# Performance work log

Measured on AMD Instinct MI355X. Metric: run time of the kernel, lower is better.

Reference implementation:

```python
import jax, jax.numpy as jnp
import numpy as np

B, T, D, R = 4, 2048, 1024, 32


def setup_inputs() -> dict:
    key = jax.random.key(0)
    kx, ku = jax.random.split(key)
    x = jax.random.normal(kx, (B, T, D), dtype=jnp.float32)
    # low-rank metric factor; small init so distances are moderate
    U = jax.random.normal(ku, (D, R), dtype=jnp.float32) * 0.05
    return {"x": x, "U": U}


def reference(x, U):
    # g = U @ U.T (PSD low-rank metric).
    # dist_sq[b,t,j] = (x_t - x_j)^T g (x_t - x_j)
    #               = ||U^T x_t||^2 + ||U^T x_j||^2 - 2 (U^T x_t).(U^T x_j)
    # Algebraic expansion of the original O(B*T*T*D) broadcasted diff tensor.
    y = jnp.einsum('btd,dr->btr', x, U)                # [B,T,R]
    n = jnp.sum(y * y, axis=-1)                         # [B,T]
    cross = jnp.einsum('btr,bjr->btj', y, y)            # [B,T,T]
    dist_sq = n[:, :, None] + n[:, None, :] - 2.0 * cross
    attn = jax.nn.softmax(-dist_sq, axis=-1)            # [B,T,T]
    return jnp.einsum('btj,bjd->btd', attn, x)          # [B,T,D]
```

## Files before the change

### kernel.cpp

```cpp
#include <hip/hip_runtime.h>

#define B_ 4
#define T_ 2048
#define D_ 1024
#define R_ 32
#define XSTR2 136

typedef __attribute__((ext_vector_type(8))) short short8;
typedef __attribute__((ext_vector_type(4))) float f32x4;
typedef __attribute__((ext_vector_type(4))) unsigned short us4;
typedef __attribute__((ext_vector_type(8))) unsigned short us8;

__device__ __forceinline__ unsigned short f2bf(float f) {
  union { float f; unsigned u; } v; v.f = f;
  unsigned r = (v.u + 0x7fffu + ((v.u >> 16) & 1u)) >> 16;
  return (unsigned short)r;
}
__device__ __forceinline__ float bf2f(unsigned short h) {
  union { unsigned u; float f; } v; v.u = (unsigned)h << 16;
  return v.f;
}

__global__ __launch_bounds__(256)
void geo_ut(const float* __restrict__ U, unsigned short* __restrict__ Ut) {
  __shared__ float tile[128][33];
  const int tid = threadIdx.x;
  const int d0 = blockIdx.x * 128;
  #pragma unroll
  for (int i = 0; i < 16; i++) {
    int e = i * 256 + tid;
    int d = e >> 5, r = e & 31;
    tile[d][r] = U[(size_t)(d0 + d) * R_ + r];
  }
  __syncthreads();
  const int r = tid >> 3, seg = tid & 7;
  us8 o0, o1;
  #pragma unroll
  for (int k = 0; k < 8; k++) o0[k] = f2bf(tile[seg * 16 + k][r]);
  #pragma unroll
  for (int k = 0; k < 8; k++) o1[k] = f2bf(tile[seg * 16 + 8 + k][r]);
  *(us8*)(Ut + (size_t)r * D_ + d0 + seg * 16) = o0;
  *(us8*)(Ut + (size_t)r * D_ + d0 + seg * 16 + 8) = o1;
}

__global__ __launch_bounds__(256)
void geo_prep(const float* __restrict__ x, const unsigned short* __restrict__ Ut,
              unsigned short* __restrict__ xt, float* __restrict__ y_part) {
  __shared__ unsigned short xs[2][32 * XSTR2];
  const int b = blockIdx.y, slab = blockIdx.z;
  const int t0 = blockIdx.x * 32;
  const int d0 = slab * 256;
  const int tid = threadIdx.x, w = tid >> 6, lane = tid & 63;
  const int m = lane & 15, quad = lane >> 4;
  const int Mt = w & 1, Nt = w >> 1;
  const int lr = tid >> 3;
  const int lc = (tid & 7) * 16;

  const float* xb = x + ((size_t)b * T_ + t0 + lr) * D_ + d0 + lc;
  float4 v[2][4];
  #pragma unroll
  for (int ch = 0; ch < 2; ch++)
    #pragma unroll
    for (int i = 0; i < 4; i++)
      v[ch][i] = *(const float4*)(xb + ch * 128 + i * 4);
  #pragma unroll
  for (int ch = 0; ch < 2; ch++)
    #pragma unroll
    for (int i = 0; i < 4; i++) {
      us4 c;
      c[0] = f2bf(v[ch][i].x); c[1] = f2bf(v[ch][i].y);
      c[2] = f2bf(v[ch][i].z); c[3] = f2bf(v[ch][i].w);
      *(us4*)&xs[ch][lr * XSTR2 + lc + i * 4] = c;
    }
  __syncthreads();
  {
    const int wd = tid >> 1, wt = (tid & 1) * 16;
    #pragma unroll
    for (int ch = 0; ch < 2; ch++) {
      us8 o0, o1;
      #pragma unroll
      for (int k = 0; k < 8; k++) {
        o0[k] = xs[ch][(wt + k) * XSTR2 + wd];
        o1[k] = xs[ch][(wt + 8 + k) * XSTR2 + wd];
      }
      unsigned short* xo = xt + ((size_t)b * D_ + d0 + ch * 128 + wd) * T_ + t0;
      *(us8*)(xo + wt) = o0;
      *(us8*)(xo + wt + 8) = o1;
    }
  }
  f32x4 acc = {0.f, 0.f, 0.f, 0.f};
  #pragma unroll
  for (int ch = 0; ch < 2; ch++)
    #pragma unroll
    for (int ks = 0; ks < 4; ks++) {
      short8 af = *(const short8*)&xs[ch][(Mt * 16 + m) * XSTR2 + ks * 32 + quad * 8];
      short8 bf = *(const short8*)(Ut + (size_t)(Nt * 16 + m) * D_ + d0 + ch * 128 + ks * 32 + quad * 8);
      acc = __builtin_amdgcn_mfma_f32_16x16x32_bf16(af, bf, acc, 0, 0, 0);
    }
  float* yp = y_part + ((size_t)(slab * B_ + b) * T_ + t0 + Mt * 16 + quad * 4) * R_ + Nt * 16 + m;
  #pragma unroll
  for (int k = 0; k < 4; k++) yp[(size_t)k * R_] = acc[k];
}

__global__ __launch_bounds__(256)
void geo_reduce(const float* __restrict__ y_part, unsigned short* __restrict__ ybf,
                float* __restrict__ nsq, float* __restrict__ l) {
  const int tid = threadIdx.x;
  const size_t row = (size_t)blockIdx.x * 32 + (tid >> 3);
  const int r0 = (tid & 7) * 4;
  f32x4 v = {0.f, 0.f, 0.f, 0.f};
  #pragma unroll
  for (int s = 0; s < 4; s++) {
    f32x4 p = *(const f32x4*)(y_part + ((size_t)s * B_ * T_ + row) * R_ + r0);
    #pragma unroll
    for (int k = 0; k < 4; k++) v[k] += p[k];
  }
  us4 pk;
  float part = 0.f;
  #pragma unroll
  for (int k = 0; k < 4; k++) {
    pk[k] = f2bf(1.41421356237f * v[k]);
    float b = bf2f(pk[k]);
    part += b * b;
  }
  *(us4*)(ybf + row * R_ + r0) = pk;
  part += __shfl_xor(part, 1, 64);
  part += __shfl_xor(part, 2, 64);
  part += __shfl_xor(part, 4, 64);
  if ((tid & 7) == 0) { nsq[row] = 0.5f * part; l[row] = 0.f; }
}

__global__ __launch_bounds__(256)
void geo_scores(const unsigned short* __restrict__ ybf,
                const float* __restrict__ nsq,
                unsigned short* __restrict__ P, float* __restrict__ l,
                int jg0, int Kslab) {
  const int b = blockIdx.z;
  const int t0 = blockIdx.x * 128;
  const int jl0 = blockIdx.y * 128;
  const int tid = threadIdx.x, w = tid >> 6, lane = tid & 63;
  const int m = lane & 15, quad = lane >> 4;
  const unsigned short* yb = ybf + (size_t)b * T_ * R_;
  const float* nb = nsq + b * T_;
  const int jw = jl0 + w * 32;
  short8 aj[2]; f32x4 njv[2];
  #pragma unroll
  for (int rb = 0; rb < 2; rb++) {
    aj[rb] = *(const short8*)(yb + (size_t)(jg0 + jw + rb * 16 + m) * R_ + quad * 8);
    njv[rb] = *(const f32x4*)(nb + jg0 + jw + rb * 16 + quad * 4);
  }
  unsigned short* Pb = P + (size_t)b * T_ * Kslab;
  short8 btn = *(const short8*)(yb + (size_t)(t0 + m) * R_ + quad * 8);
  float ntn = nb[t0 + m];
  #pragma unroll 2
  for (int cb = 0; cb < 8; cb++) {
    const int t = t0 + cb * 16 + m;
    short8 bt = btn;
    float nt = ntn;
    if (cb < 7) {
      btn = *(const short8*)(yb + (size_t)(t + 16) * R_ + quad * 8);
      ntn = nb[t + 16];
    }
    float ls = 0.f;
    #pragma unroll
    for (int rb = 0; rb < 2; rb++) {
      f32x4 z = {0.f, 0.f, 0.f, 0.f};
      f32x4 c = __builtin_amdgcn_mfma_f32_16x16x32_bf16(aj[rb], bt, z, 0, 0, 0);
      us4 pk;
      #pragma unroll
      for (int r = 0; r < 4; r++) {
        float p = __expf(c[r] - njv[rb][r] - nt);
        ls += p;
        pk[r] = f2bf(p);
      }
      *(us4*)(Pb + (size_t)t * Kslab + jw + rb * 16 + quad * 4) = pk;
    }
    ls += __shfl_xor(ls, 16, 64);
    ls += __shfl_xor(ls, 32, 64);
    if (quad == 0) atomicAdd(&l[b * T_ + t], ls);
  }
}

__global__ __launch_bounds__(256)
void geo_pv(const unsigned short* __restrict__ P,
            const unsigned short* __restrict__ xt,
            const float* __restrict__ l, float* __restrict__ out,
            int Kslab, int kxt0, int accumulate, int normalize) {
  __shared__ unsigned short As[128 * 64];
  __shared__ unsigned short Bs[128 * 64];
  const int b = blockIdx.z;
  const int id = blockIdx.x;
  const int cls = id & 7, kk = id >> 3;
  const int t0 = (2 * cls + (kk >> 3)) * 128;
  const int d0 = (kk & 7) * 128;
  const int tid = threadIdx.x, w = tid >> 6, lane = tid & 63;
  const int m = lane & 15, quad = lane >> 4;
  const int wr = (w & 1) * 64, wc = (w >> 1) * 64;
  const int srow = lane >> 3, sslot = lane & 7;
  const unsigned short* Pb = P + ((size_t)b * T_ + t0) * Kslab;
  const unsigned short* Xb = xt + ((size_t)b * D_ + d0) * T_ + kxt0;
  f32x4 acc[4][4];
  #pragma unroll
  for (int i = 0; i < 4; i++)
    #pragma unroll
    for (int j = 0; j < 4; j++) acc[i][j] = (f32x4){0.f, 0.f, 0.f, 0.f};

  for (int k0 = 0; k0 < Kslab; k0 += 64) {
    __syncthreads();
    #pragma unroll
    for (int cc = 0; cc < 4; cc++) {
      const int row = w * 32 + cc * 8 + srow;
      const int gs = sslot ^ (row & 7);
      __builtin_amdgcn_global_load_lds(
          (const __attribute__((address_space(1))) void*)(Pb + (size_t)row * Kslab + k0 + gs * 8),
          (__attribute__((address_space(3))) void*)(As + (w * 32 + cc * 8) * 64),
          16, 0, 0);
      __builtin_amdgcn_global_load_lds(
          (const __attribute__((address_space(1))) void*)(Xb + (size_t)row * T_ + k0 + gs * 8),
          (__attribute__((address_space(3))) void*)(Bs + (w * 32 + cc * 8) * 64),
          16, 0, 0);
    }
    __syncthreads();
    #pragma unroll
    for (int ks = 0; ks < 2; ks++) {
      short8 af[4], bf[4];
      #pragma unroll
      for (int i = 0; i < 4; i++) {
        const int ra = wr + i * 16 + m;
        af[i] = *(const short8*)(As + ra * 64 + (((ks * 4 + quad) ^ (m & 7)) * 8));
        const int cd = wc + i * 16 + m;
        bf[i] = *(const short8*)(Bs + cd * 64 + (((ks * 4 + quad) ^ (m & 7)) * 8));
      }
      #pragma unroll
      for (int rb = 0; rb < 4; rb++)
        #pragma unroll
        for (int cb = 0; cb < 4; cb++)
          acc[rb][cb] = __builtin_amdgcn_mfma_f32_16x16x32_bf16(af[rb], bf[cb], acc[rb][cb], 0, 0, 0);
    }
  }
  float* ob = out + ((size_t)b * T_ + t0 + wr) * D_ + d0 + wc;
  #pragma unroll
  for (int rb = 0; rb < 4; rb++) {
    f32x4 lv = *(const f32x4*)(l + b * T_ + t0 + wr + rb * 16 + quad * 4);
    f32x4 inv;
    #pragma unroll
    for (int r = 0; r < 4; r++) inv[r] = 1.f / lv[r];
    #pragma unroll
    for (int cb = 0; cb < 4; cb++) {
      #pragma unroll
      for (int r = 0; r < 4; r++) {
        float* p = ob + (size_t)(rb * 16 + quad * 4 + r) * D_ + cb * 16 + m;
        float v = acc[rb][cb][r];
        if (accumulate) v += *p;
        if (normalize) v *= inv[r];
        *p = v;
      }
    }
  }
}

extern "C" void kernel_launch(void* const* d_in, const int* in_sizes, int n_in,
                              void* d_out, int out_size, void* d_ws, size_t ws_size,
                              hipStream_t stream) {
  const float* x = (const float*)d_in[0];
  const float* U = (const float*)d_in[1];
  float* out = (float*)d_out;

  const size_t xt_b  = (size_t)B_ * D_ * T_ * 2;
  const size_t ybf_b = (size_t)B_ * T_ * R_ * 2;
  const size_t nsq_b = (size_t)B_ * T_ * 4;
  const size_t l_b   = nsq_b;
  const size_t ut_b  = (size_t)D_ * R_ * 2;
  const size_t yp_b  = (size_t)4 * B_ * T_ * R_ * 4;
  const size_t base  = xt_b + ybf_b + nsq_b + l_b + ut_b + yp_b;
  const size_t pfull = (size_t)B_ * T_ * T_ * 2;

  int nslab = 16;
  const int cand[5] = {1, 2, 4, 8, 16};
  for (int i = 0; i < 5; i++)
    if (base + pfull / (size_t)cand[i] <= ws_size) { nslab = cand[i]; break; }
  const int Kslab = T_ / nslab;

  char* wp = (char*)d_ws;
  unsigned short* xtp = (unsigned short*)wp;                 wp += xt_b;
  unsigned short* ybf = (unsigned short*)wp;                 wp += ybf_b;
  float* nsq = (float*)wp;                                   wp += nsq_b;
  float* lp  = (float*)wp;                                   wp += l_b;
  unsigned short* Utp = (unsigned short*)wp;                 wp += ut_b;
  float* ypart = (float*)wp;                                 wp += yp_b;
  unsigned short* P = (unsigned short*)wp;

  hipLaunchKernelGGL(geo_ut, dim3(D_ / 128), dim3(256), 0, stream, U, Utp);
  hipLaunchKernelGGL(geo_prep, dim3(T_ / 32, B_, 4), dim3(256), 0, stream,
                     x, Utp, xtp, ypart);
  hipLaunchKernelGGL(geo_reduce, dim3(B_ * T_ / 32), dim3(256), 0, stream,
                     ypart, ybf, nsq, lp);
  for (int s = 0; s < nslab; s++) {
    hipLaunchKernelGGL(geo_scores, dim3(T_ / 128, Kslab / 128, B_), dim3(256), 0, stream,
                       ybf, nsq, P, lp, s * Kslab, Kslab);
    hipLaunchKernelGGL(geo_pv, dim3(128, 1, B_), dim3(256), 0, stream,
                       P, xtp, lp, out, Kslab, s * Kslab,
                       (int)(s > 0), (int)(s == nslab - 1));
  }
}
```

Before: 156.5 us.

## Fuse score computation and softmax into PV GEMM, dropping materialized P matrix

Replaces the separate scores kernel, which wrote a bf16 probability matrix to global memory, with a single fused kernel. That kernel recomputes the exp scores per 64-column tile straight into shared memory and feeds them to the PV MFMA loop. Row sums are accumulated in registers and normalization happens in the epilogue, which removes the atomics, the P round trip and the multi-slab launches. The y vectors are prescaled by sqrt(2/ln2) so that exp2 can be used. The cost is that each of the eight d-tile blocks per t-tile recomputes the same scores, which adds redundant MFMA and exp work.

```diff
diff --git a/kernel.cpp b/kernel.cpp
--- a/kernel.cpp
+++ b/kernel.cpp
@@ -104,7 +104,7 @@
 
 __global__ __launch_bounds__(256)
 void geo_reduce(const float* __restrict__ y_part, unsigned short* __restrict__ ybf,
-                float* __restrict__ nsq, float* __restrict__ l) {
+                float* __restrict__ nsq) {
   const int tid = threadIdx.x;
   const size_t row = (size_t)blockIdx.x * 32 + (tid >> 3);
   const int r0 = (tid & 7) * 4;
@@ -119,7 +119,7 @@
   float part = 0.f;
   #pragma unroll
   for (int k = 0; k < 4; k++) {
-    pk[k] = f2bf(1.41421356237f * v[k]);
+    pk[k] = f2bf(1.69864446f * v[k]);
     float b = bf2f(pk[k]);
     part += b * b;
   }
@@ -127,98 +127,92 @@
   part += __shfl_xor(part, 1, 64);
   part += __shfl_xor(part, 2, 64);
   part += __shfl_xor(part, 4, 64);
-  if ((tid & 7) == 0) { nsq[row] = 0.5f * part; l[row] = 0.f; }
-}
-
-__global__ __launch_bounds__(256)
-void geo_scores(const unsigned short* __restrict__ ybf,
-                const float* __restrict__ nsq,
-                unsigned short* __restrict__ P, float* __restrict__ l,
-                int jg0, int Kslab) {
-  const int b = blockIdx.z;
-  const int t0 = blockIdx.x * 128;
-  const int jl0 = blockIdx.y * 128;
-  const int tid = threadIdx.x, w = tid >> 6, lane = tid & 63;
-  const int m = lane & 15, quad = lane >> 4;
-  const unsigned short* yb = ybf + (size_t)b * T_ * R_;
-  const float* nb = nsq + b * T_;
-  const int jw = jl0 + w * 32;
-  short8 aj[2]; f32x4 njv[2];
-  #pragma unroll
-  for (int rb = 0; rb < 2; rb++) {
-    aj[rb] = *(const short8*)(yb + (size_t)(jg0 + jw + rb * 16 + m) * R_ + quad * 8);
-    njv[rb] = *(const f32x4*)(nb + jg0 + jw + rb * 16 + quad * 4);
-  }
-  unsigned short* Pb = P + (size_t)b * T_ * Kslab;
-  short8 btn = *(const short8*)(yb + (size_t)(t0 + m) * R_ + quad * 8);
-  float ntn = nb[t0 + m];
-  #pragma unroll 2
-  for (int cb = 0; cb < 8; cb++) {
-    const int t = t0 + cb * 16 + m;
-    short8 bt = btn;
-    float nt = ntn;
-    if (cb < 7) {
-      btn = *(const short8*)(yb + (size_t)(t + 16) * R_ + quad * 8);
-      ntn = nb[t + 16];
-    }
-    float ls = 0.f;
-    #pragma unroll
-    for (int rb = 0; rb < 2; rb++) {
-      f32x4 z = {0.f, 0.f, 0.f, 0.f};
-      f32x4 c = __builtin_amdgcn_mfma_f32_16x16x32_bf16(aj[rb], bt, z, 0, 0, 0);
-      us4 pk;
-      #pragma unroll
-      for (int r = 0; r < 4; r++) {
-        float p = __expf(c[r] - njv[rb][r] - nt);
-        ls += p;
-        pk[r] = f2bf(p);
-      }
-      *(us4*)(Pb + (size_t)t * Kslab + jw + rb * 16 + quad * 4) = pk;
-    }
-    ls += __shfl_xor(ls, 16, 64);
-    ls += __shfl_xor(ls, 32, 64);
-    if (quad == 0) atomicAdd(&l[b * T_ + t], ls);
-  }
-}
-
-__global__ __launch_bounds__(256)
-void geo_pv(const unsigned short* __restrict__ P,
-            const unsigned short* __restrict__ xt,
-            const float* __restrict__ l, float* __restrict__ out,
-            int Kslab, int kxt0, int accumulate, int normalize) {
+  if ((tid & 7) == 0) nsq[row] = 0.5f * part;
+}
+
+__global__ __launch_bounds__(256, 2)
+void geo_fused(const unsigned short* __restrict__ ybf,
+               const float* __restrict__ nsq,
+               const unsigned short* __restrict__ xt,
+               float* __restrict__ out) {
   __shared__ unsigned short As[128 * 64];
   __shared__ unsigned short Bs[128 * 64];
+  __shared__ float l_s[128];
   const int b = blockIdx.z;
   const int id = blockIdx.x;
-  const int cls = id & 7, kk = id >> 3;
-  const int t0 = (2 * cls + (kk >> 3)) * 128;
-  const int d0 = (kk & 7) * 128;
+  const int d0 = (id & 7) * 128;
+  const int t0 = (id >> 3) * 128;
   const int tid = threadIdx.x, w = tid >> 6, lane = tid & 63;
   const int m = lane & 15, quad = lane >> 4;
   const int wr = (w & 1) * 64, wc = (w >> 1) * 64;
   const int srow = lane >> 3, sslot = lane & 7;
-  const unsigned short* Pb = P + ((size_t)b * T_ + t0) * Kslab;
-  const unsigned short* Xb = xt + ((size_t)b * D_ + d0) * T_ + kxt0;
+  const int tw = w * 32;
+
+  const unsigned short* yb = ybf + (size_t)b * T_ * R_;
+  const float* nb = nsq + b * T_;
+  const unsigned short* Xb = xt + ((size_t)b * D_ + d0) * T_;
+
+  short8 at[2]; float nnt[2]; float lsum[2] = {0.f, 0.f};
+  #pragma unroll
+  for (int tb = 0; tb < 2; tb++) {
+    at[tb] = *(const short8*)(yb + (size_t)(t0 + tw + tb * 16 + m) * R_ + quad * 8);
+    nnt[tb] = -nb[t0 + tw + tb * 16 + m];
+  }
+
   f32x4 acc[4][4];
   #pragma unroll
   for (int i = 0; i < 4; i++)
     #pragma unroll
     for (int j = 0; j < 4; j++) acc[i][j] = (f32x4){0.f, 0.f, 0.f, 0.f};
 
-  for (int k0 = 0; k0 < Kslab; k0 += 64) {
+  short8 aj[4]; f32x4 njv[4];
+  #pragma unroll
+  for (int ja = 0; ja < 4; ja++) {
+    aj[ja] = *(const short8*)(yb + (size_t)(ja * 16 + m) * R_ + quad * 8);
+    njv[ja] = *(const f32x4*)(nb + ja * 16 + quad * 4);
+  }
+
+  for (int j0 = 0; j0 < T_; j0 += 64) {
     __syncthreads();
     #pragma unroll
     for (int cc = 0; cc < 4; cc++) {
       const int row = w * 32 + cc * 8 + srow;
       const int gs = sslot ^ (row & 7);
       __builtin_amdgcn_global_load_lds(
-          (const __attribute__((address_space(1))) void*)(Pb + (size_t)row * Kslab + k0 + gs * 8),
-          (__attribute__((address_space(3))) void*)(As + (w * 32 + cc * 8) * 64),
-          16, 0, 0);
-      __builtin_amdgcn_global_load_lds(
-          (const __attribute__((address_space(1))) void*)(Xb + (size_t)row * T_ + k0 + gs * 8),
+          (const __attribute__((address_space(1))) void*)(Xb + (size_t)row * T_ + j0 + gs * 8),
           (__attribute__((address_space(3))) void*)(Bs + (w * 32 + cc * 8) * 64),
           16, 0, 0);
+    }
+    short8 caj[4]; f32x4 cnj[4];
+    #pragma unroll
+    for (int ja = 0; ja < 4; ja++) { caj[ja] = aj[ja]; cnj[ja] = njv[ja]; }
+    const int jn = (j0 + 64 < T_) ? j0 + 64 : 0;
+    #pragma unroll
+    for (int ja = 0; ja < 4; ja++) {
+      aj[ja] = *(const short8*)(yb + (size_t)(jn + ja * 16 + m) * R_ + quad * 8);
+      njv[ja] = *(const f32x4*)(nb + jn + ja * 16 + quad * 4);
+    }
+    #pragma unroll
+    for (int tb = 0; tb < 2; tb++) {
+      const int trow = tw + tb * 16 + m;
+      #pragma unroll
+      for (int ja = 0; ja < 4; ja++) {
+        f32x4 cin;
+        #pragma unroll
+        for (int r = 0; r < 4; r++) cin[r] = nnt[tb] - cnj[ja][r];
+        f32x4 c = __builtin_amdgcn_mfma_f32_16x16x32_bf16(caj[ja], at[tb], cin, 0, 0, 0);
+        us4 pk; float ls = 0.f;
+        #pragma unroll
+        for (int r = 0; r < 4; r++) {
+          float p = __builtin_amdgcn_exp2f(c[r]);
+          ls += p;
+          pk[r] = f2bf(p);
+        }
+        lsum[tb] += ls;
+        const int sb = ja * 2 + (quad >> 1);
+        char* dst = (char*)As + trow * 128 + ((sb ^ (trow & 7)) * 16) + (quad & 1) * 8;
+        *(us4*)dst = pk;
+      }
     }
     __syncthreads();
     #pragma unroll
@@ -238,24 +232,25 @@
           acc[rb][cb] = __builtin_amdgcn_mfma_f32_16x16x32_bf16(af[rb], bf[cb], acc[rb][cb], 0, 0, 0);
     }
   }
+  #pragma unroll
+  for (int tb = 0; tb < 2; tb++) {
+    lsum[tb] += __shfl_xor(lsum[tb], 16, 64);
+    lsum[tb] += __shfl_xor(lsum[tb], 32, 64);
+  }
+  if (quad == 0) { l_s[tw + m] = lsum[0]; l_s[tw + 16 + m] = lsum[1]; }
+  __syncthreads();
   float* ob = out + ((size_t)b * T_ + t0 + wr) * D_ + d0 + wc;
   #pragma unroll
   for (int rb = 0; rb < 4; rb++) {
-    f32x4 lv = *(const f32x4*)(l + b * T_ + t0 + wr + rb * 16 + quad * 4);
+    f32x4 lv = *(const f32x4*)&l_s[wr + rb * 16 + quad * 4];
     f32x4 inv;
     #pragma unroll
     for (int r = 0; r < 4; r++) inv[r] = 1.f / lv[r];
     #pragma unroll
-    for (int cb = 0; cb < 4; cb++) {
-      #pragma unroll
-      for (int r = 0; r < 4; r++) {
-        float* p = ob + (size_t)(rb * 16 + quad * 4 + r) * D_ + cb * 16 + m;
-        float v = acc[rb][cb][r];
-        if (accumulate) v += *p;
-        if (normalize) v *= inv[r];
-        *p = v;
-      }
-    }
+    for (int cb = 0; cb < 4; cb++)
+      #pragma unroll
+      for (int r = 0; r < 4; r++)
+        ob[(size_t)(rb * 16 + quad * 4 + r) * D_ + cb * 16 + m] = acc[rb][cb][r] * inv[r];
   }
 }
 
@@ -269,37 +264,22 @@
   const size_t xt_b  = (size_t)B_ * D_ * T_ * 2;
   const size_t ybf_b = (size_t)B_ * T_ * R_ * 2;
   const size_t nsq_b = (size_t)B_ * T_ * 4;
-  const size_t l_b   = nsq_b;
   const size_t ut_b  = (size_t)D_ * R_ * 2;
   const size_t yp_b  = (size_t)4 * B_ * T_ * R_ * 4;
-  const size_t base  = xt_b + ybf_b + nsq_b + l_b + ut_b + yp_b;
-  const size_t pfull = (size_t)B_ * T_ * T_ * 2;
-
-  int nslab = 16;
-  const int cand[5] = {1, 2, 4, 8, 16};
-  for (int i = 0; i < 5; i++)
-    if (base + pfull / (size_t)cand[i] <= ws_size) { nslab = cand[i]; break; }
-  const int Kslab = T_ / nslab;
 
   char* wp = (char*)d_ws;
   unsigned short* xtp = (unsigned short*)wp;                 wp += xt_b;
   unsigned short* ybf = (unsigned short*)wp;                 wp += ybf_b;
   float* nsq = (float*)wp;                                   wp += nsq_b;
-  float* lp  = (float*)wp;                                   wp += l_b;
   unsigned short* Utp = (unsigned short*)wp;                 wp += ut_b;
   float* ypart = (float*)wp;                                 wp += yp_b;
-  unsigned short* P = (unsigned short*)wp;
+  (void)ws_size; (void)in_sizes; (void)n_in; (void)out_size;
 
   hipLaunchKernelGGL(geo_ut, dim3(D_ / 128), dim3(256), 0, stream, U, Utp);
   hipLaunchKernelGGL(geo_prep, dim3(T_ / 32, B_, 4), dim3(256), 0, stream,
                      x, Utp, xtp, ypart);
   hipLaunchKernelGGL(geo_reduce, dim3(B_ * T_ / 32), dim3(256), 0, stream,
-                     ypart, ybf, nsq, lp);
-  for (int s = 0; s < nslab; s++) {
-    hipLaunchKernelGGL(geo_scores, dim3(T_ / 128, Kslab / 128, B_), dim3(256), 0, stream,
-                       ybf, nsq, P, lp, s * Kslab, Kslab);
-    hipLaunchKernelGGL(geo_pv, dim3(128, 1, B_), dim3(256), 0, stream,
-                       P, xtp, lp, out, Kslab, s * Kslab,
-                       (int)(s > 0), (int)(s == nslab - 1));
-  }
-}
+                     ypart, ybf, nsq);
+  hipLaunchKernelGGL(geo_fused, dim3((T_ / 128) * (D_ / 128), 1, B_), dim3(256), 0, stream,
+                     ybf, nsq, xtp, out);
+}
```

Measured after the change: 155.3 us. Within noise of the previous version (-0.8%).
